# Kernel optimization log

Hardware: AMD Instinct MI355X
Metric: run time of the kernel (lower is better)

Reference implementation:

```python
import jax, jax.numpy as jnp
import numpy as np

DIM = 192
NUM_HEADS = 6
WH, WW = 7, 7
N = WH * WW  # 49 tokens per window
C2 = 2 * DIM  # concatenated channel dim = 384
SCALE = (DIM // NUM_HEADS) ** -0.5  # module uses dim//num_heads, not C2//num_heads
NW = 64  # number of windows per image
B_ = 2048  # num_windows * batch


def _relative_position_index():
    ch = np.arange(WH)
    cw = np.arange(WW)
    coords = np.stack(np.meshgrid(ch, cw, indexing='ij')).reshape(2, -1)  # [2, N]
    rel = coords[:, :, None] - coords[:, None, :]  # [2, N, N]
    rel = rel.transpose(1, 2, 0).astype(np.int64)  # [N, N, 2]
    rel[..., 0] += WH - 1
    rel[..., 1] += WW - 1
    rel[..., 0] *= 2 * WW - 1
    return jnp.asarray(rel.sum(-1))  # [N, N]

REL_IDX = _relative_position_index()


def setup_inputs() -> dict:
    key = jax.random.key(0)
    ks = jax.random.split(key, 8)
    x = jax.random.normal(ks[0], (B_, N, DIM), dtype=jnp.float32)
    y = jax.random.normal(ks[1], (B_, N, DIM), dtype=jnp.float32)
    mask = jax.random.normal(ks[2], (NW, N, N), dtype=jnp.float32)
    w_qkv = jax.random.normal(ks[3], (6 * DIM, C2), dtype=jnp.float32) * 0.02
    b_qkv = jnp.zeros((6 * DIM,), dtype=jnp.float32)
    w_proj = jax.random.normal(ks[4], (DIM, C2), dtype=jnp.float32) * 0.02
    b_proj = jnp.zeros((DIM,), dtype=jnp.float32)
    bias_table = jax.random.normal(ks[5], ((2 * WH - 1) * (2 * WW - 1), NUM_HEADS), dtype=jnp.float32) * 0.02
    return {"x": x, "y": y, "mask": mask, "w_qkv": w_qkv, "b_qkv": b_qkv,
            "w_proj": w_proj, "b_proj": b_proj, "bias_table": bias_table}


def reference(x, y, mask, w_qkv, b_qkv, w_proj, b_proj, bias_table):
    Bc = x.shape[0]
    Dh = C2 // NUM_HEADS  # 64
    xy = jnp.concatenate([x, y], axis=2)  # [B_, N, 2*dim]
    qkv = xy @ w_qkv.T + b_qkv  # [B_, N, 6*dim]
    qkv = qkv.reshape(Bc, N, 3, NUM_HEADS, Dh).transpose(2, 0, 3, 1, 4)  # [3, B_, H, N, Dh]
    q, k, v = qkv[0] * SCALE, qkv[1], qkv[2]
    attn = jnp.einsum('bhnd,bhmd->bhnm', q, k)  # [B_, H, N, N]
    rpb = bias_table[REL_IDX]  # [N, N, H]
    attn = attn + rpb.transpose(2, 0, 1)[None]
    nW = mask.shape[0]
    attn = attn.reshape(Bc // nW, nW, NUM_HEADS, N, N) + mask[None, :, None]
    attn = attn.reshape(Bc, NUM_HEADS, N, N)
    attn = jax.nn.softmax(attn, axis=-1)
    out = jnp.einsum('bhnm,bhmd->bhnd', attn, v)  # [B_, H, N, Dh]
    out = out.transpose(0, 2, 1, 3).reshape(Bc, N, C2)
    return out @ w_proj.T + b_proj  # [B_, N, dim]
```

## Files before the change

kernel.cpp:

```cpp
#include <hip/hip_runtime.h>
#include <hip/hip_bf16.h>


typedef __attribute__((ext_vector_type(8))) short short8;
typedef __attribute__((ext_vector_type(4))) float f32x4;

#define SCALE 0.17677669529663687f

#define WQF_OFF    0ul
#define WQF_BYTES  (864ul*1024)
#define WPF_OFF    (WQF_OFF + WQF_BYTES)
#define WPF_BYTES  (144ul*1024)
#define COMB_OFF   (WPF_OFF + WPF_BYTES)
#define COMB_BYTES (64ul*6*4096*4)
#define XYF_OFF    (COMB_OFF + COMB_BYTES)
#define XYF_BYTES  (2048ul*48*1024)
#define OF_OFF     (XYF_OFF + XYF_BYTES)
#define OF_BYTES   XYF_BYTES
#define WS_NEED    (OF_OFF + OF_BYTES)

__device__ __forceinline__ unsigned short f2bf(float f){
  unsigned u = __builtin_bit_cast(unsigned, f);
  u = u + 0x7fffu + ((u >> 16) & 1u);
  return (unsigned short)(u >> 16);
}
__device__ __forceinline__ unsigned long long pack4(float4 v){
  return (unsigned long long)f2bf(v.x) | ((unsigned long long)f2bf(v.y) << 16)
       | ((unsigned long long)f2bf(v.z) << 32) | ((unsigned long long)f2bf(v.w) << 48);
}

__device__ __forceinline__ unsigned short cvt1(float x){
  unsigned r;
  asm("v_cvt_pk_bf16_f32 %0, %1, %1" : "=v"(r) : "v"(x));
  return (unsigned short)r;
}
__device__ __forceinline__ uint2 pk4(float a, float b, float c, float d){
  unsigned lo, hi;
  asm("v_cvt_pk_bf16_f32 %0, %1, %2" : "=v"(lo) : "v"(a), "v"(b));
  asm("v_cvt_pk_bf16_f32 %0, %1, %2" : "=v"(hi) : "v"(c), "v"(d));
  return make_uint2(lo, hi);
}

__global__ void k0_wfrag(const float* __restrict__ wq_f, const float* __restrict__ wp_f,
                         unsigned short* __restrict__ wqf, unsigned short* __restrict__ wpf){
  int t = blockIdx.x*256 + threadIdx.x;
  int fragidx = t >> 6, l = t & 63;
  const float* src; unsigned short* dst;
  float sc = 1.0f;
  if (fragidx < 864){
    int h = fragidx/144, rem = fragidx - h*144;
    int ct = rem/12, kt = rem - ct*12;
    int row = (ct>>2)*384 + h*64 + (ct&3)*16 + (l&15);
    src = wq_f + (long)row*384 + kt*32 + (l>>4)*8;
    dst = wqf + (long)fragidx*512 + l*8;
    if (ct < 4) sc = SCALE;
  } else {
    int fid = fragidx - 864;
    int ct = fid/12, kt = fid - ct*12;
    int row = ct*16 + (l&15);
    src = wp_f + (long)row*384 + kt*32 + (l>>4)*8;
    dst = wpf + (long)fid*512 + l*8;
  }
  short8 v;
  #pragma unroll
  for (int e = 0; e < 8; ++e) v[e] = (short)f2bf(src[e] * sc);
  *(short8*)dst = v;
}

__global__ void prep_comb(const float* __restrict__ mask, const float* __restrict__ btab,
                          float* __restrict__ comb){
  int idx = blockIdx.x * 256 + threadIdx.x;
  int j = idx & 63, i = (idx >> 6) & 63, rest = idx >> 12;
  int h = rest % 6, w = rest / 6;
  float v;
  if (i < 49 && j < 49){
    int di = i / 7 - j / 7 + 6;
    int dj = i % 7 - j % 7 + 6;
    v = btab[(di * 13 + dj) * 6 + h] + mask[(w * 49 + i) * 49 + j];
  } else {
    v = (j >= 49) ? -1e30f : 0.0f;
  }
  comb[idx] = v;
}

__global__ void k1_xyfrag(const float* __restrict__ x, const float* __restrict__ y,
                          unsigned short* __restrict__ xyf){
  const int kt  = blockIdx.x;
  const int win = blockIdx.y;
  const int mt  = threadIdx.x >> 6;
  const int l   = threadIdx.x & 63;
  const int row = mt*16 + (l & 15);
  const int c0  = kt*32 + (l >> 4)*8;
  short8 v = {};
  if (row < 49){
    const float* src = (kt < 6) ? (x + ((long)win*49 + row)*192 + c0)
                                : (y + ((long)win*49 + row)*192 + (c0 - 192));
    float4 f0 = *(const float4*)src, f1 = *(const float4*)(src+4);
    unsigned long long lo = pack4(f0), hi = pack4(f1);
    #pragma unroll
    for (int e = 0; e < 4; ++e){ v[e] = (short)(lo >> (16*e)); v[4+e] = (short)(hi >> (16*e)); }
  }
  *(short8*)(xyf + (((long)win*12 + kt)*4 + mt)*512 + l*8) = v;
}

__device__ __forceinline__ int swz(int r, int b){ return b ^ ((r & 7) << 4); }
__device__ __forceinline__ int a_q (int r, int c){ return 0     + swz(r, r*128 + c*2); }
__device__ __forceinline__ int a_k (int r, int c){ return 8192  + swz(r, r*128 + c*2); }
__device__ __forceinline__ int a_vt(int r, int c){ return 16384 + swz(r, r*128 + c*2); }

__global__ __launch_bounds__(256, 3)
void k2_qkv_attn(const unsigned short* __restrict__ xyf, const unsigned short* __restrict__ wqf,
                 const float* __restrict__ bqkv, const float* __restrict__ comb,
                 unsigned short* __restrict__ Of){
  __shared__ __align__(16) unsigned char smem[24576];
  const int h = blockIdx.x, win = blockIdx.y;
  const int tid = threadIdx.x, w = tid>>6, l = tid&63, l15 = l&15, lg = l>>4;

  float bias[3];
  #pragma unroll
  for (int nt = 0; nt < 3; ++nt){
    int ct = w*3 + nt, s = ct >> 2;
    bias[nt] = bqkv[s*384 + h*64 + (ct & 3)*16 + l15];
    if (s == 0) bias[nt] *= SCALE;
  }

  const unsigned short* Ab = xyf + (long)win*24576;
  const unsigned short* Bb = wqf + ((long)h*12 + w*3)*12*512;
  short8 aA[2][4], bB[2][3];
  #pragma unroll
  for (int mt = 0; mt < 4; ++mt) aA[0][mt] = *(const short8*)(Ab + mt*512 + l*8);
  #pragma unroll
  for (int nt = 0; nt < 3; ++nt) bB[0][nt] = *(const short8*)(Bb + (nt*12)*512 + l*8);

  f32x4 acc[4][3];
  #pragma unroll
  for (int mt = 0; mt < 4; ++mt)
    #pragma unroll
    for (int nt = 0; nt < 3; ++nt)
      #pragma unroll
      for (int j = 0; j < 4; ++j) acc[mt][nt][j] = bias[nt];

  #pragma unroll
  for (int kt = 0; kt < 12; ++kt){
    const int cur = kt & 1, nxt = cur ^ 1;
    if (kt < 11){
      #pragma unroll
      for (int mt = 0; mt < 4; ++mt)
        aA[nxt][mt] = *(const short8*)(Ab + ((kt+1)*4 + mt)*512 + l*8);
      #pragma unroll
      for (int nt = 0; nt < 3; ++nt)
        bB[nxt][nt] = *(const short8*)(Bb + (nt*12 + kt+1)*512 + l*8);
    }
    __builtin_amdgcn_sched_barrier(0);
    __builtin_amdgcn_s_setprio(1);
    #pragma unroll
    for (int nt = 0; nt < 3; ++nt){
      #pragma unroll
      for (int mt = 0; mt < 4; ++mt)
        acc[mt][nt] = __builtin_amdgcn_mfma_f32_16x16x32_bf16(aA[cur][mt], bB[cur][nt], acc[mt][nt], 0, 0, 0);
    }
    __builtin_amdgcn_s_setprio(0);
  }

  const float* cb = comb + ((long)((win & 63)*6 + h))*4096 + (w*16 + l15)*64 + lg*4;
  float4 cbv[4];
  #pragma unroll
  for (int nt = 0; nt < 4; ++nt) cbv[nt] = *(const float4*)(cb + nt*16);

  #pragma unroll
  for (int nt = 0; nt < 3; ++nt){
    int ct = w*3 + nt, s = ct >> 2, d16 = (ct & 3) * 16;
    if (s == 2){
      #pragma unroll
      for (int mt = 0; mt < 4; ++mt){
        uint2 p = pk4(acc[mt][nt][0], acc[mt][nt][1], acc[mt][nt][2], acc[mt][nt][3]);
        *(uint2*)(smem + a_vt(d16 + l15, mt*16 + lg*4)) = p;
      }
    } else {
      #pragma unroll
      for (int mt = 0; mt < 4; ++mt){
        #pragma unroll
        for (int j = 0; j < 4; ++j){
          int row = mt*16 + lg*4 + j;
          int addr = (s == 0) ? a_q(row, d16 + l15) : a_k(row, d16 + l15);
          *(unsigned short*)(smem + addr) = cvt1(acc[mt][nt][j]);
        }
      }
    }
  }
  __syncthreads();

  short8 bq[2];
  #pragma unroll
  for (int ks = 0; ks < 2; ++ks)
    bq[ks] = *(const short8*)(smem + a_q(w*16 + l15, ks*32 + lg*8));
  f32x4 st[4] = {};
  __builtin_amdgcn_s_setprio(1);
  #pragma unroll
  for (int ks = 0; ks < 2; ++ks){
    #pragma unroll
    for (int nt = 0; nt < 4; ++nt){
      short8 ak = *(const short8*)(smem + a_k(nt*16 + l15, ks*32 + lg*8));
      st[nt] = __builtin_amdgcn_mfma_f32_16x16x32_bf16(ak, bq[ks], st[nt], 0, 0, 0);
    }
  }
  __builtin_amdgcn_s_setprio(0);
  #pragma unroll
  for (int nt = 0; nt < 4; ++nt){
    st[nt][0] += cbv[nt].x; st[nt][1] += cbv[nt].y;
    st[nt][2] += cbv[nt].z; st[nt][3] += cbv[nt].w;
  }
  float mx;
  {
    float m0 = fmaxf(fmaxf(st[0][0], st[0][1]), fmaxf(st[0][2], st[0][3]));
    float m1 = fmaxf(fmaxf(st[1][0], st[1][1]), fmaxf(st[1][2], st[1][3]));
    float m2 = fmaxf(fmaxf(st[2][0], st[2][1]), fmaxf(st[2][2], st[2][3]));
    float m3 = fmaxf(fmaxf(st[3][0], st[3][1]), fmaxf(st[3][2], st[3][3]));
    mx = fmaxf(fmaxf(m0, m1), fmaxf(m2, m3));
  }
  mx = fmaxf(mx, __shfl_xor(mx, 16));
  mx = fmaxf(mx, __shfl_xor(mx, 32));
  float ssum = 0.f;
  #pragma unroll
  for (int nt = 0; nt < 4; ++nt){
    #pragma unroll
    for (int j = 0; j < 4; ++j){
      float e = __expf(st[nt][j] - mx);
      st[nt][j] = e; ssum += e;
    }
  }
  ssum += __shfl_xor(ssum, 16);
  ssum += __shfl_xor(ssum, 32);
  const float inv = 1.0f / ssum;

  #pragma unroll
  for (int nt = 0; nt < 4; ++nt){
    uint2 p = pk4(st[nt][0]*inv, st[nt][1]*inv, st[nt][2]*inv, st[nt][3]*inv);
    *(uint2*)(smem + a_q(w*16 + l15, nt*16 + lg*4)) = p;
  }

  short8 ap[2];
  #pragma unroll
  for (int ks = 0; ks < 2; ++ks)
    ap[ks] = *(const short8*)(smem + a_q(w*16 + l15, ks*32 + lg*8));
  f32x4 oacc[4] = {};
  __builtin_amdgcn_s_setprio(1);
  #pragma unroll
  for (int ks = 0; ks < 2; ++ks){
    #pragma unroll
    for (int nt = 0; nt < 4; ++nt){
      short8 bv = *(const short8*)(smem + a_vt(nt*16 + l15, ks*32 + lg*8));
      oacc[nt] = __builtin_amdgcn_mfma_f32_16x16x32_bf16(ap[ks], bv, oacc[nt], 0, 0, 0);
    }
  }
  __builtin_amdgcn_s_setprio(0);
  #pragma unroll
  for (int nt = 0; nt < 4; ++nt){
    #pragma unroll
    for (int j = 0; j < 4; ++j)
      *(unsigned short*)(smem + a_q(w*16 + lg*4 + j, nt*16 + l15)) = cvt1(oacc[nt][j]);
  }
  unsigned short* Ob = Of + (((long)win*12 + h*2)*4 + w)*512 + l*8;
  #pragma unroll
  for (int ks = 0; ks < 2; ++ks){
    short8 o8 = *(const short8*)(smem + a_q(w*16 + l15, ks*32 + lg*8));
    *(short8*)(Ob + ks*4*512) = o8;
  }
}

__global__ __launch_bounds__(256, 3)
void k3_proj(const unsigned short* __restrict__ Of, const unsigned short* __restrict__ wpf,
             const float* __restrict__ bproj, float* __restrict__ out){
  const int win = blockIdx.x;
  const int tid = threadIdx.x, w = tid>>6, l = tid&63, l15 = l&15, lg = l>>4;
  float bp[3]; int np[3];
  #pragma unroll
  for (int nt = 0; nt < 3; ++nt){
    np[nt] = w*48 + nt*16 + l15;
    bp[nt] = bproj[np[nt]];
  }
  const unsigned short* Ab = Of + (long)win*24576;
  const unsigned short* Bb = wpf + (long)(w*3)*12*512;
  short8 aA[2][4], bB[2][3];
  #pragma unroll
  for (int mt = 0; mt < 4; ++mt) aA[0][mt] = *(const short8*)(Ab + mt*512 + l*8);
  #pragma unroll
  for (int nt = 0; nt < 3; ++nt) bB[0][nt] = *(const short8*)(Bb + (nt*12)*512 + l*8);
  f32x4 acc[4][3];
  #pragma unroll
  for (int mt = 0; mt < 4; ++mt)
    #pragma unroll
    for (int nt = 0; nt < 3; ++nt)
      #pragma unroll
      for (int j = 0; j < 4; ++j) acc[mt][nt][j] = bp[nt];
  #pragma unroll
  for (int kt = 0; kt < 12; ++kt){
    const int cur = kt & 1, nxt = cur ^ 1;
    if (kt < 11){
      #pragma unroll
      for (int mt = 0; mt < 4; ++mt)
        aA[nxt][mt] = *(const short8*)(Ab + ((kt+1)*4 + mt)*512 + l*8);
      #pragma unroll
      for (int nt = 0; nt < 3; ++nt)
        bB[nxt][nt] = *(const short8*)(Bb + (nt*12 + kt+1)*512 + l*8);
    }
    __builtin_amdgcn_sched_barrier(0);
    __builtin_amdgcn_s_setprio(1);
    #pragma unroll
    for (int nt = 0; nt < 3; ++nt){
      #pragma unroll
      for (int mt = 0; mt < 4; ++mt)
        acc[mt][nt] = __builtin_amdgcn_mfma_f32_16x16x32_bf16(aA[cur][mt], bB[cur][nt], acc[mt][nt], 0, 0, 0);
    }
    __builtin_amdgcn_s_setprio(0);
  }
  #pragma unroll
  for (int mt = 0; mt < 4; ++mt){
    #pragma unroll
    for (int j = 0; j < 4; ++j){
      int row = mt*16 + lg*4 + j;
      if (row < 49){
        float* o = out + ((long)win*49 + row)*192;
        #pragma unroll
        for (int nt = 0; nt < 3; ++nt)
          o[np[nt]] = acc[mt][nt][j];
      }
    }
  }
}

#define FB_WQ_ELEMS (1152*384)
#define FB_WP_ELEMS (192*384)
#define FB_WP_OFF   (FB_WQ_ELEMS*2)
#define FB_COMB_OFF (FB_WP_OFF + FB_WP_ELEMS*2)

__global__ void prep_weights_fb(const float* __restrict__ wq_f, const float* __restrict__ wp_f,
                                unsigned short* __restrict__ wq, unsigned short* __restrict__ wp){
  int gid = blockIdx.x * 256 + threadIdx.x;
  if (gid < FB_WQ_ELEMS) wq[gid] = f2bf(wq_f[gid]);
  else { int g = gid - FB_WQ_ELEMS; if (g < FB_WP_ELEMS) wp[g] = f2bf(wp_f[g]); }
}
__device__ __forceinline__ int fb_xy(int r, int c){ return 0      + swz(r, r*768 + c*2); }
__device__ __forceinline__ int fb_q (int r, int c){ return 49152  + swz(r, r*128 + c*2); }
__device__ __forceinline__ int fb_k (int r, int c){ return 57344  + swz(r, r*128 + c*2); }
__device__ __forceinline__ int fb_vt(int r, int c){ return 65536  + swz(r, r*128 + c*2); }
__device__ __forceinline__ int fb_p (int r, int c){ return 73728  + swz(r, r*128 + c*2); }

__global__ __launch_bounds__(256, 2)
void fused_attn_fb(const float* __restrict__ x, const float* __restrict__ y,
                   const float* __restrict__ bqkv, const float* __restrict__ bproj,
                   const unsigned short* __restrict__ wq, const unsigned short* __restrict__ wp,
                   const float* __restrict__ comb, float* __restrict__ out){
  __shared__ __align__(16) unsigned char smem[81920];
  const int b = blockIdx.x, tid = threadIdx.x;
  const int w = tid>>6, l = tid&63, l15 = l&15, lg = l>>4;
  {
    const float4* x4 = (const float4*)x + b * 2352;
    const float4* y4 = (const float4*)y + b * 2352;
    for (int idx = tid; idx < 2352; idx += 256){
      int r = idx / 48, c4 = (idx % 48) * 4;
      float4 vx = x4[idx], vy = y4[idx];
      *(unsigned long long*)(smem + fb_xy(r, c4))       = pack4(vx);
      *(unsigned long long*)(smem + fb_xy(r, 192 + c4)) = pack4(vy);
    }
    for (int idx = tid; idx < 1440; idx += 256){
      int r = 49 + idx / 96, c4 = (idx % 96) * 4;
      *(unsigned long long*)(smem + fb_xy(r, c4)) = 0ull;
    }
  }
  __syncthreads();
  const float* cbB = comb + (long)(b & 63) * (6 * 4096);
  f32x4 pacc[4][3] = {};
  int np[3]; float bp[3];
  #pragma unroll
  for (int nt = 0; nt < 3; ++nt){ np[nt] = w*48 + nt*16 + l15; bp[nt] = bproj[np[nt]]; }
  #pragma unroll 1
  for (int h = 0; h < 6; ++h){
    f32x4 acc[4][3] = {};
    int wrow[3]; float bias[3];
    #pragma unroll
    for (int nt = 0; nt < 3; ++nt){
      int n = np[nt];
      wrow[nt] = (n >> 6) * 384 + h * 64 + (n & 63);
      bias[nt] = bqkv[wrow[nt]];
    }
    #pragma unroll 4
    for (int kt = 0; kt < 12; ++kt){
      int k0 = kt * 32;
      short8 a[4];
      #pragma unroll
      for (int mt = 0; mt < 4; ++mt)
        a[mt] = *(const short8*)(smem + fb_xy(mt*16 + l15, k0 + lg*8));
      #pragma unroll
      for (int nt = 0; nt < 3; ++nt){
        short8 bb = *(const short8*)(wq + (long)wrow[nt]*384 + k0 + lg*8);
        #pragma unroll
        for (int mt = 0; mt < 4; ++mt)
          acc[mt][nt] = __builtin_amdgcn_mfma_f32_16x16x32_bf16(a[mt], bb, acc[mt][nt], 0, 0, 0);
      }
    }
    #pragma unroll
    for (int nt = 0; nt < 3; ++nt){
      int n = np[nt], s = n >> 6, d = n & 63;
      #pragma unroll
      for (int mt = 0; mt < 4; ++mt){
        #pragma unroll
        for (int j = 0; j < 4; ++j){
          int row = mt*16 + lg*4 + j;
          float v = acc[mt][nt][j] + bias[nt];
          if (s == 0) v *= SCALE;
          int addr = (s==0) ? fb_q(row,d) : (s==1) ? fb_k(row,d) : fb_vt(d,row);
          *(unsigned short*)(smem + addr) = f2bf(v);
        }
      }
    }
    __syncthreads();
    short8 aq[2];
    #pragma unroll
    for (int ks = 0; ks < 2; ++ks)
      aq[ks] = *(const short8*)(smem + fb_q(w*16 + l15, ks*32 + lg*8));
    f32x4 sacc[4] = {};
    #pragma unroll
    for (int ks = 0; ks < 2; ++ks)
      #pragma unroll
      for (int nt = 0; nt < 4; ++nt){
        short8 bk = *(const short8*)(smem + fb_k(nt*16 + l15, ks*32 + lg*8));
        sacc[nt] = __builtin_amdgcn_mfma_f32_16x16x32_bf16(aq[ks], bk, sacc[nt], 0, 0, 0);
      }
    const float* cb = cbB + h * 4096;
    float rs[4];
    #pragma unroll
    for (int j = 0; j < 4; ++j){
      int r = w*16 + lg*4 + j;
      #pragma unroll
      for (int nt = 0; nt < 4; ++nt) sacc[nt][j] += cb[r*64 + nt*16 + l15];
      float m = fmaxf(fmaxf(sacc[0][j], sacc[1][j]), fmaxf(sacc[2][j], sacc[3][j]));
      #pragma unroll
      for (int dlt = 1; dlt < 16; dlt <<= 1) m = fmaxf(m, __shfl_xor(m, dlt));
      float ssum = 0.f;
      #pragma unroll
      for (int nt = 0; nt < 4; ++nt){
        float e = __expf(sacc[nt][j] - m);
        sacc[nt][j] = e; ssum += e;
      }
      #pragma unroll
      for (int dlt = 1; dlt < 16; dlt <<= 1) ssum += __shfl_xor(ssum, dlt);
      rs[j] = ssum;
      #pragma unroll
      for (int nt = 0; nt < 4; ++nt)
        *(unsigned short*)(smem + fb_p(r, nt*16 + l15)) = f2bf(sacc[nt][j]);
    }
    short8 ap[2];
    #pragma unroll
    for (int ks = 0; ks < 2; ++ks)
      ap[ks] = *(const short8*)(smem + fb_p(w*16 + l15, ks*32 + lg*8));
    f32x4 oacc[4] = {};
    #pragma unroll
    for (int ks = 0; ks < 2; ++ks)
      #pragma unroll
      for (int nt = 0; nt < 4; ++nt){
        short8 bv = *(const short8*)(smem + fb_vt(nt*16 + l15, ks*32 + lg*8));
        oacc[nt] = __builtin_amdgcn_mfma_f32_16x16x32_bf16(ap[ks], bv, oacc[nt], 0, 0, 0);
      }
    float inv[4];
    #pragma unroll
    for (int j = 0; j < 4; ++j) inv[j] = 1.0f / rs[j];
    #pragma unroll
    for (int nt = 0; nt < 4; ++nt)
      #pragma unroll
      for (int j = 0; j < 4; ++j){
        int row = w*16 + lg*4 + j;
        *(unsigned short*)(smem + fb_p(row, nt*16 + l15)) = f2bf(oacc[nt][j] * inv[j]);
      }
    __syncthreads();
    #pragma unroll
    for (int ks = 0; ks < 2; ++ks){
      short8 ao8[4];
      #pragma unroll
      for (int mt = 0; mt < 4; ++mt)
        ao8[mt] = *(const short8*)(smem + fb_p(mt*16 + l15, ks*32 + lg*8));
      #pragma unroll
      for (int nt = 0; nt < 3; ++nt){
        short8 bb = *(const short8*)(wp + (long)np[nt]*384 + h*64 + ks*32 + lg*8);
        #pragma unroll
        for (int mt = 0; mt < 4; ++mt)
          pacc[mt][nt] = __builtin_amdgcn_mfma_f32_16x16x32_bf16(ao8[mt], bb, pacc[mt][nt], 0, 0, 0);
      }
    }
  }
  #pragma unroll
  for (int mt = 0; mt < 4; ++mt)
    #pragma unroll
    for (int j = 0; j < 4; ++j){
      int row = mt*16 + lg*4 + j;
      if (row < 49){
        float* o = out + ((long)b*49 + row)*192;
        #pragma unroll
        for (int nt = 0; nt < 3; ++nt)
          o[np[nt]] = pacc[mt][nt][j] + bp[nt];
      }
    }
}

extern "C" void kernel_launch(void* const* d_in, const int* in_sizes, int n_in,
                              void* d_out, int out_size, void* d_ws, size_t ws_size,
                              hipStream_t stream){
  (void)in_sizes; (void)n_in; (void)out_size;
  const float* x     = (const float*)d_in[0];
  const float* y     = (const float*)d_in[1];
  const float* mask  = (const float*)d_in[2];
  const float* wq_f  = (const float*)d_in[3];
  const float* bqkv  = (const float*)d_in[4];
  const float* wp_f  = (const float*)d_in[5];
  const float* bproj = (const float*)d_in[6];
  const float* btab  = (const float*)d_in[7];
  float* out = (float*)d_out;

  if (ws_size >= WS_NEED){
    unsigned short* wqf = (unsigned short*)((char*)d_ws + WQF_OFF);
    unsigned short* wpf = (unsigned short*)((char*)d_ws + WPF_OFF);
    float*          cmb = (float*)((char*)d_ws + COMB_OFF);
    unsigned short* xyf = (unsigned short*)((char*)d_ws + XYF_OFF);
    unsigned short* Ofr = (unsigned short*)((char*)d_ws + OF_OFF);
    hipLaunchKernelGGL(k0_wfrag,    dim3(252),     dim3(256), 0, stream, wq_f, wp_f, wqf, wpf);
    hipLaunchKernelGGL(prep_comb,   dim3(6144),    dim3(256), 0, stream, mask, btab, cmb);
    hipLaunchKernelGGL(k1_xyfrag,   dim3(12,2048), dim3(256), 0, stream, x, y, xyf);
    hipLaunchKernelGGL(k2_qkv_attn, dim3(6,2048),  dim3(256), 0, stream, xyf, wqf, bqkv, cmb, Ofr);
    hipLaunchKernelGGL(k3_proj,     dim3(2048),    dim3(256), 0, stream, Ofr, wpf, bproj, out);
  } else {
    unsigned short* wq  = (unsigned short*)d_ws;
    unsigned short* wp  = (unsigned short*)((char*)d_ws + FB_WP_OFF);
    float*          cmb = (float*)((char*)d_ws + FB_COMB_OFF);
    hipLaunchKernelGGL(prep_weights_fb, dim3(2016), dim3(256), 0, stream, wq_f, wp_f, wq, wp);
    hipLaunchKernelGGL(prep_comb,       dim3(6144), dim3(256), 0, stream, mask, btab, cmb);
    hipLaunchKernelGGL(fused_attn_fb,   dim3(2048), dim3(256), 0, stream,
                       x, y, bqkv, bproj, wq, wp, cmb, out);
  }
}
```

Baseline: 251.6 us.

## Fuse input conversion, per-head QKV attention and projection into one kernel per window

```diff
diff --git a/kernel.cpp b/kernel.cpp
--- a/kernel.cpp
+++ b/kernel.cpp
@@ -13,11 +13,7 @@
 #define WPF_BYTES  (144ul*1024)
 #define COMB_OFF   (WPF_OFF + WPF_BYTES)
 #define COMB_BYTES (64ul*6*4096*4)
-#define XYF_OFF    (COMB_OFF + COMB_BYTES)
-#define XYF_BYTES  (2048ul*48*1024)
-#define OF_OFF     (XYF_OFF + XYF_BYTES)
-#define OF_BYTES   XYF_BYTES
-#define WS_NEED    (OF_OFF + OF_BYTES)
+#define WS_NEED    (COMB_OFF + COMB_BYTES)
 
 __device__ __forceinline__ unsigned short f2bf(float f){
   unsigned u = __builtin_bit_cast(unsigned, f);
@@ -83,237 +79,229 @@
   comb[idx] = v;
 }
 
-__global__ void k1_xyfrag(const float* __restrict__ x, const float* __restrict__ y,
-                          unsigned short* __restrict__ xyf){
-  const int kt  = blockIdx.x;
-  const int win = blockIdx.y;
-  const int mt  = threadIdx.x >> 6;
-  const int l   = threadIdx.x & 63;
-  const int row = mt*16 + (l & 15);
-  const int c0  = kt*32 + (l >> 4)*8;
-  short8 v = {};
-  if (row < 49){
-    const float* src = (kt < 6) ? (x + ((long)win*49 + row)*192 + c0)
-                                : (y + ((long)win*49 + row)*192 + (c0 - 192));
-    float4 f0 = *(const float4*)src, f1 = *(const float4*)(src+4);
-    unsigned long long lo = pack4(f0), hi = pack4(f1);
-    #pragma unroll
-    for (int e = 0; e < 4; ++e){ v[e] = (short)(lo >> (16*e)); v[4+e] = (short)(hi >> (16*e)); }
-  }
-  *(short8*)(xyf + (((long)win*12 + kt)*4 + mt)*512 + l*8) = v;
-}
-
 __device__ __forceinline__ int swz(int r, int b){ return b ^ ((r & 7) << 4); }
-__device__ __forceinline__ int a_q (int r, int c){ return 0     + swz(r, r*128 + c*2); }
-__device__ __forceinline__ int a_k (int r, int c){ return 8192  + swz(r, r*128 + c*2); }
-__device__ __forceinline__ int a_vt(int r, int c){ return 16384 + swz(r, r*128 + c*2); }
-
-__global__ __launch_bounds__(256, 3)
-void k2_qkv_attn(const unsigned short* __restrict__ xyf, const unsigned short* __restrict__ wqf,
-                 const float* __restrict__ bqkv, const float* __restrict__ comb,
-                 unsigned short* __restrict__ Of){
-  __shared__ __align__(16) unsigned char smem[24576];
-  const int h = blockIdx.x, win = blockIdx.y;
-  const int tid = threadIdx.x, w = tid>>6, l = tid&63, l15 = l&15, lg = l>>4;
-
-  float bias[3];
-  #pragma unroll
-  for (int nt = 0; nt < 3; ++nt){
-    int ct = w*3 + nt, s = ct >> 2;
-    bias[nt] = bqkv[s*384 + h*64 + (ct & 3)*16 + l15];
-    if (s == 0) bias[nt] *= SCALE;
-  }
-
-  const unsigned short* Ab = xyf + (long)win*24576;
-  const unsigned short* Bb = wqf + ((long)h*12 + w*3)*12*512;
-  short8 aA[2][4], bB[2][3];
-  #pragma unroll
-  for (int mt = 0; mt < 4; ++mt) aA[0][mt] = *(const short8*)(Ab + mt*512 + l*8);
-  #pragma unroll
-  for (int nt = 0; nt < 3; ++nt) bB[0][nt] = *(const short8*)(Bb + (nt*12)*512 + l*8);
-
-  f32x4 acc[4][3];
-  #pragma unroll
-  for (int mt = 0; mt < 4; ++mt)
-    #pragma unroll
-    for (int nt = 0; nt < 3; ++nt)
-      #pragma unroll
-      for (int j = 0; j < 4; ++j) acc[mt][nt][j] = bias[nt];
-
-  #pragma unroll
-  for (int kt = 0; kt < 12; ++kt){
-    const int cur = kt & 1, nxt = cur ^ 1;
-    if (kt < 11){
-      #pragma unroll
-      for (int mt = 0; mt < 4; ++mt)
-        aA[nxt][mt] = *(const short8*)(Ab + ((kt+1)*4 + mt)*512 + l*8);
-      #pragma unroll
-      for (int nt = 0; nt < 3; ++nt)
-        bB[nxt][nt] = *(const short8*)(Bb + (nt*12 + kt+1)*512 + l*8);
-    }
-    __builtin_amdgcn_sched_barrier(0);
-    __builtin_amdgcn_s_setprio(1);
-    #pragma unroll
-    for (int nt = 0; nt < 3; ++nt){
-      #pragma unroll
-      for (int mt = 0; mt < 4; ++mt)
-        acc[mt][nt] = __builtin_amdgcn_mfma_f32_16x16x32_bf16(aA[cur][mt], bB[cur][nt], acc[mt][nt], 0, 0, 0);
-    }
-    __builtin_amdgcn_s_setprio(0);
-  }
-
-  const float* cb = comb + ((long)((win & 63)*6 + h))*4096 + (w*16 + l15)*64 + lg*4;
-  float4 cbv[4];
-  #pragma unroll
-  for (int nt = 0; nt < 4; ++nt) cbv[nt] = *(const float4*)(cb + nt*16);
-
-  #pragma unroll
-  for (int nt = 0; nt < 3; ++nt){
-    int ct = w*3 + nt, s = ct >> 2, d16 = (ct & 3) * 16;
-    if (s == 2){
-      #pragma unroll
-      for (int mt = 0; mt < 4; ++mt){
-        uint2 p = pk4(acc[mt][nt][0], acc[mt][nt][1], acc[mt][nt][2], acc[mt][nt][3]);
-        *(uint2*)(smem + a_vt(d16 + l15, mt*16 + lg*4)) = p;
-      }
-    } else {
-      #pragma unroll
-      for (int mt = 0; mt < 4; ++mt){
-        #pragma unroll
-        for (int j = 0; j < 4; ++j){
-          int row = mt*16 + lg*4 + j;
-          int addr = (s == 0) ? a_q(row, d16 + l15) : a_k(row, d16 + l15);
-          *(unsigned short*)(smem + addr) = cvt1(acc[mt][nt][j]);
-        }
-      }
-    }
-  }
-  __syncthreads();
-
-  short8 bq[2];
-  #pragma unroll
-  for (int ks = 0; ks < 2; ++ks)
-    bq[ks] = *(const short8*)(smem + a_q(w*16 + l15, ks*32 + lg*8));
-  f32x4 st[4] = {};
-  __builtin_amdgcn_s_setprio(1);
-  #pragma unroll
-  for (int ks = 0; ks < 2; ++ks){
-    #pragma unroll
-    for (int nt = 0; nt < 4; ++nt){
-      short8 ak = *(const short8*)(smem + a_k(nt*16 + l15, ks*32 + lg*8));
-      st[nt] = __builtin_amdgcn_mfma_f32_16x16x32_bf16(ak, bq[ks], st[nt], 0, 0, 0);
-    }
-  }
-  __builtin_amdgcn_s_setprio(0);
-  #pragma unroll
-  for (int nt = 0; nt < 4; ++nt){
-    st[nt][0] += cbv[nt].x; st[nt][1] += cbv[nt].y;
-    st[nt][2] += cbv[nt].z; st[nt][3] += cbv[nt].w;
-  }
-  float mx;
-  {
-    float m0 = fmaxf(fmaxf(st[0][0], st[0][1]), fmaxf(st[0][2], st[0][3]));
-    float m1 = fmaxf(fmaxf(st[1][0], st[1][1]), fmaxf(st[1][2], st[1][3]));
-    float m2 = fmaxf(fmaxf(st[2][0], st[2][1]), fmaxf(st[2][2], st[2][3]));
-    float m3 = fmaxf(fmaxf(st[3][0], st[3][1]), fmaxf(st[3][2], st[3][3]));
-    mx = fmaxf(fmaxf(m0, m1), fmaxf(m2, m3));
-  }
-  mx = fmaxf(mx, __shfl_xor(mx, 16));
-  mx = fmaxf(mx, __shfl_xor(mx, 32));
-  float ssum = 0.f;
-  #pragma unroll
-  for (int nt = 0; nt < 4; ++nt){
-    #pragma unroll
-    for (int j = 0; j < 4; ++j){
-      float e = __expf(st[nt][j] - mx);
-      st[nt][j] = e; ssum += e;
-    }
-  }
-  ssum += __shfl_xor(ssum, 16);
-  ssum += __shfl_xor(ssum, 32);
-  const float inv = 1.0f / ssum;
-
-  #pragma unroll
-  for (int nt = 0; nt < 4; ++nt){
-    uint2 p = pk4(st[nt][0]*inv, st[nt][1]*inv, st[nt][2]*inv, st[nt][3]*inv);
-    *(uint2*)(smem + a_q(w*16 + l15, nt*16 + lg*4)) = p;
-  }
-
-  short8 ap[2];
-  #pragma unroll
-  for (int ks = 0; ks < 2; ++ks)
-    ap[ks] = *(const short8*)(smem + a_q(w*16 + l15, ks*32 + lg*8));
-  f32x4 oacc[4] = {};
-  __builtin_amdgcn_s_setprio(1);
-  #pragma unroll
-  for (int ks = 0; ks < 2; ++ks){
-    #pragma unroll
-    for (int nt = 0; nt < 4; ++nt){
-      short8 bv = *(const short8*)(smem + a_vt(nt*16 + l15, ks*32 + lg*8));
-      oacc[nt] = __builtin_amdgcn_mfma_f32_16x16x32_bf16(ap[ks], bv, oacc[nt], 0, 0, 0);
-    }
-  }
-  __builtin_amdgcn_s_setprio(0);
-  #pragma unroll
-  for (int nt = 0; nt < 4; ++nt){
-    #pragma unroll
-    for (int j = 0; j < 4; ++j)
-      *(unsigned short*)(smem + a_q(w*16 + lg*4 + j, nt*16 + l15)) = cvt1(oacc[nt][j]);
-  }
-  unsigned short* Ob = Of + (((long)win*12 + h*2)*4 + w)*512 + l*8;
-  #pragma unroll
-  for (int ks = 0; ks < 2; ++ks){
-    short8 o8 = *(const short8*)(smem + a_q(w*16 + l15, ks*32 + lg*8));
-    *(short8*)(Ob + ks*4*512) = o8;
-  }
-}
-
-__global__ __launch_bounds__(256, 3)
-void k3_proj(const unsigned short* __restrict__ Of, const unsigned short* __restrict__ wpf,
-             const float* __restrict__ bproj, float* __restrict__ out){
+__device__ __forceinline__ int a_q (int r, int c){ return 49152 + swz(r, r*128 + c*2); }
+__device__ __forceinline__ int a_k (int r, int c){ return 57344 + swz(r, r*128 + c*2); }
+__device__ __forceinline__ int a_vt(int r, int c){ return 65536 + swz(r, r*128 + c*2); }
+#define OBUF 73728
+
+__global__ __launch_bounds__(256, 2)
+void k_fused(const float* __restrict__ x, const float* __restrict__ y,
+             const unsigned short* __restrict__ wqf, const unsigned short* __restrict__ wpf,
+             const float* __restrict__ bqkv, const float* __restrict__ bproj,
+             const float* __restrict__ comb, float* __restrict__ out){
+  __shared__ __align__(16) unsigned char smem[81920];
   const int win = blockIdx.x;
   const int tid = threadIdx.x, w = tid>>6, l = tid&63, l15 = l&15, lg = l>>4;
-  float bp[3]; int np[3];
+
+  for (int t = tid; t < 2352; t += 256){
+    int r = t / 48, c8 = t - r*48;
+    int c = c8*8;
+    const float* src = (c < 192) ? (x + ((long)win*49 + r)*192 + c)
+                                 : (y + ((long)win*49 + r)*192 + (c - 192));
+    float4 f0 = *(const float4*)src, f1 = *(const float4*)(src + 4);
+    uint2 lo = pk4(f0.x, f0.y, f0.z, f0.w);
+    uint2 hi = pk4(f1.x, f1.y, f1.z, f1.w);
+    uint4 vv = make_uint4(lo.x, lo.y, hi.x, hi.y);
+    int addr = (c8>>2)*4096 + (r>>4)*1024 + (((r&15) + (c8&3)*16))*16;
+    *(uint4*)(smem + addr) = vv;
+  }
+  for (int t = tid; t < 720; t += 256){
+    int rr = t / 48, c8 = t - rr*48;
+    int r = 49 + rr;
+    int addr = (c8>>2)*4096 + (r>>4)*1024 + (((r&15) + (c8&3)*16))*16;
+    *(uint4*)(smem + addr) = make_uint4(0,0,0,0);
+  }
+
+  int np[3];
+  f32x4 pacc[4][3];
   #pragma unroll
   for (int nt = 0; nt < 3; ++nt){
     np[nt] = w*48 + nt*16 + l15;
-    bp[nt] = bproj[np[nt]];
-  }
-  const unsigned short* Ab = Of + (long)win*24576;
-  const unsigned short* Bb = wpf + (long)(w*3)*12*512;
-  short8 aA[2][4], bB[2][3];
+    float bv = bproj[np[nt]];
+    #pragma unroll
+    for (int mt = 0; mt < 4; ++mt)
+      #pragma unroll
+      for (int j = 0; j < 4; ++j) pacc[mt][nt][j] = (mt == 0 && j == 0) ? bv : ((mt==0&&j==0)?bv:0.0f);
+  }
   #pragma unroll
-  for (int mt = 0; mt < 4; ++mt) aA[0][mt] = *(const short8*)(Ab + mt*512 + l*8);
-  #pragma unroll
-  for (int nt = 0; nt < 3; ++nt) bB[0][nt] = *(const short8*)(Bb + (nt*12)*512 + l*8);
-  f32x4 acc[4][3];
-  #pragma unroll
-  for (int mt = 0; mt < 4; ++mt)
-    #pragma unroll
-    for (int nt = 0; nt < 3; ++nt)
-      #pragma unroll
-      for (int j = 0; j < 4; ++j) acc[mt][nt][j] = bp[nt];
-  #pragma unroll
-  for (int kt = 0; kt < 12; ++kt){
-    const int cur = kt & 1, nxt = cur ^ 1;
-    if (kt < 11){
+  for (int nt = 0; nt < 3; ++nt){
+    float bv = bproj[np[nt]];
+    #pragma unroll
+    for (int mt = 0; mt < 4; ++mt)
+      #pragma unroll
+      for (int j = 0; j < 4; ++j) pacc[mt][nt][j] = bv;
+  }
+
+  __syncthreads();
+
+  #pragma unroll 1
+  for (int h = 0; h < 6; ++h){
+    const float* cb = comb + ((long)((win & 63)*6 + h))*4096 + (w*16 + l15)*64 + lg*4;
+    float4 cbv[4];
+    #pragma unroll
+    for (int nt = 0; nt < 4; ++nt) cbv[nt] = *(const float4*)(cb + nt*16);
+
+    float bias[3];
+    #pragma unroll
+    for (int nt = 0; nt < 3; ++nt){
+      int ct = w*3 + nt, s = ct >> 2;
+      bias[nt] = bqkv[s*384 + h*64 + (ct & 3)*16 + l15];
+      if (s == 0) bias[nt] *= SCALE;
+    }
+
+    const unsigned short* Bb = wqf + ((long)h*12 + w*3)*12*512;
+    short8 bB[2][3];
+    #pragma unroll
+    for (int nt = 0; nt < 3; ++nt) bB[0][nt] = *(const short8*)(Bb + (nt*12)*512 + l*8);
+    f32x4 acc[4][3];
+    #pragma unroll
+    for (int mt = 0; mt < 4; ++mt)
+      #pragma unroll
+      for (int nt = 0; nt < 3; ++nt)
+        #pragma unroll
+        for (int j = 0; j < 4; ++j) acc[mt][nt][j] = bias[nt];
+
+    #pragma unroll
+    for (int kt = 0; kt < 12; ++kt){
+      const int cur = kt & 1, nxt = cur ^ 1;
+      if (kt < 11){
+        #pragma unroll
+        for (int nt = 0; nt < 3; ++nt)
+          bB[nxt][nt] = *(const short8*)(Bb + (nt*12 + kt+1)*512 + l*8);
+      }
+      short8 aA[4];
       #pragma unroll
       for (int mt = 0; mt < 4; ++mt)
-        aA[nxt][mt] = *(const short8*)(Ab + ((kt+1)*4 + mt)*512 + l*8);
-      #pragma unroll
-      for (int nt = 0; nt < 3; ++nt)
-        bB[nxt][nt] = *(const short8*)(Bb + (nt*12 + kt+1)*512 + l*8);
-    }
-    __builtin_amdgcn_sched_barrier(0);
+        aA[mt] = *(const short8*)(smem + (kt*4 + mt)*1024 + l*16);
+      __builtin_amdgcn_sched_barrier(0);
+      __builtin_amdgcn_s_setprio(1);
+      #pragma unroll
+      for (int nt = 0; nt < 3; ++nt){
+        #pragma unroll
+        for (int mt = 0; mt < 4; ++mt)
+          acc[mt][nt] = __builtin_amdgcn_mfma_f32_16x16x32_bf16(aA[mt], bB[cur][nt], acc[mt][nt], 0, 0, 0);
+      }
+      __builtin_amdgcn_s_setprio(0);
+    }
+
+    #pragma unroll
+    for (int nt = 0; nt < 3; ++nt){
+      int ct = w*3 + nt, s = ct >> 2, d16 = (ct & 3) * 16;
+      if (s == 2){
+        #pragma unroll
+        for (int mt = 0; mt < 4; ++mt){
+          uint2 p = pk4(acc[mt][nt][0], acc[mt][nt][1], acc[mt][nt][2], acc[mt][nt][3]);
+          *(uint2*)(smem + a_vt(d16 + l15, mt*16 + lg*4)) = p;
+        }
+      } else {
+        #pragma unroll
+        for (int mt = 0; mt < 4; ++mt){
+          #pragma unroll
+          for (int j = 0; j < 4; ++j){
+            int row = mt*16 + lg*4 + j;
+            int addr = (s == 0) ? a_q(row, d16 + l15) : a_k(row, d16 + l15);
+            *(unsigned short*)(smem + addr) = cvt1(acc[mt][nt][j]);
+          }
+        }
+      }
+    }
+    __syncthreads();
+
+    short8 bq[2];
+    #pragma unroll
+    for (int ks = 0; ks < 2; ++ks)
+      bq[ks] = *(const short8*)(smem + a_q(w*16 + l15, ks*32 + lg*8));
+    f32x4 st[4] = {};
     __builtin_amdgcn_s_setprio(1);
     #pragma unroll
-    for (int nt = 0; nt < 3; ++nt){
+    for (int ks = 0; ks < 2; ++ks){
+      #pragma unroll
+      for (int nt = 0; nt < 4; ++nt){
+        short8 ak = *(const short8*)(smem + a_k(nt*16 + l15, ks*32 + lg*8));
+        st[nt] = __builtin_amdgcn_mfma_f32_16x16x32_bf16(ak, bq[ks], st[nt], 0, 0, 0);
+      }
+    }
+    __builtin_amdgcn_s_setprio(0);
+    #pragma unroll
+    for (int nt = 0; nt < 4; ++nt){
+      st[nt][0] += cbv[nt].x; st[nt][1] += cbv[nt].y;
+      st[nt][2] += cbv[nt].z; st[nt][3] += cbv[nt].w;
+    }
+    float mx;
+    {
+      float m0 = fmaxf(fmaxf(st[0][0], st[0][1]), fmaxf(st[0][2], st[0][3]));
+      float m1 = fmaxf(fmaxf(st[1][0], st[1][1]), fmaxf(st[1][2], st[1][3]));
+      float m2 = fmaxf(fmaxf(st[2][0], st[2][1]), fmaxf(st[2][2], st[2][3]));
+      float m3 = fmaxf(fmaxf(st[3][0], st[3][1]), fmaxf(st[3][2], st[3][3]));
+      mx = fmaxf(fmaxf(m0, m1), fmaxf(m2, m3));
+    }
+    mx = fmaxf(mx, __shfl_xor(mx, 16));
+    mx = fmaxf(mx, __shfl_xor(mx, 32));
+    float ssum = 0.f;
+    #pragma unroll
+    for (int nt = 0; nt < 4; ++nt){
+      #pragma unroll
+      for (int j = 0; j < 4; ++j){
+        float e = __expf(st[nt][j] - mx);
+        st[nt][j] = e; ssum += e;
+      }
+    }
+    ssum += __shfl_xor(ssum, 16);
+    ssum += __shfl_xor(ssum, 32);
+    const float inv = 1.0f / ssum;
+
+    #pragma unroll
+    for (int nt = 0; nt < 4; ++nt){
+      uint2 p = pk4(st[nt][0]*inv, st[nt][1]*inv, st[nt][2]*inv, st[nt][3]*inv);
+      *(uint2*)(smem + a_q(w*16 + l15, nt*16 + lg*4)) = p;
+    }
+
+    short8 ap[2];
+    #pragma unroll
+    for (int ks = 0; ks < 2; ++ks)
+      ap[ks] = *(const short8*)(smem + a_q(w*16 + l15, ks*32 + lg*8));
+    f32x4 oacc[4] = {};
+    __builtin_amdgcn_s_setprio(1);
+    #pragma unroll
+    for (int ks = 0; ks < 2; ++ks){
+      #pragma unroll
+      for (int nt = 0; nt < 4; ++nt){
+        short8 bv = *(const short8*)(smem + a_vt(nt*16 + l15, ks*32 + lg*8));
+        oacc[nt] = __builtin_amdgcn_mfma_f32_16x16x32_bf16(ap[ks], bv, oacc[nt], 0, 0, 0);
+      }
+    }
+    __builtin_amdgcn_s_setprio(0);
+    #pragma unroll
+    for (int nt = 0; nt < 4; ++nt){
+      int frag  = (nt >> 1)*4 + w;
+      int chunk0 = (lg*4) + ((nt & 1)*2 + (l15 >> 3))*16;
+      #pragma unroll
+      for (int j = 0; j < 4; ++j){
+        int addr = OBUF + frag*1024 + (chunk0 + j)*16 + (l15 & 7)*2;
+        *(unsigned short*)(smem + addr) = cvt1(oacc[nt][j]);
+      }
+    }
+    __syncthreads();
+
+    #pragma unroll
+    for (int ks = 0; ks < 2; ++ks){
+      short8 aO[4];
       #pragma unroll
       for (int mt = 0; mt < 4; ++mt)
-        acc[mt][nt] = __builtin_amdgcn_mfma_f32_16x16x32_bf16(aA[cur][mt], bB[cur][nt], acc[mt][nt], 0, 0, 0);
-    }
-    __builtin_amdgcn_s_setprio(0);
-  }
+        aO[mt] = *(const short8*)(smem + OBUF + (ks*4 + mt)*1024 + l*16);
+      __builtin_amdgcn_s_setprio(1);
+      #pragma unroll
+      for (int nt = 0; nt < 3; ++nt){
+        short8 bb = *(const short8*)(wpf + ((long)(w*3 + nt)*12 + h*2 + ks)*512 + l*8);
+        #pragma unroll
+        for (int mt = 0; mt < 4; ++mt)
+          pacc[mt][nt] = __builtin_amdgcn_mfma_f32_16x16x32_bf16(aO[mt], bb, pacc[mt][nt], 0, 0, 0);
+      }
+      __builtin_amdgcn_s_setprio(0);
+    }
+  }
+
   #pragma unroll
   for (int mt = 0; mt < 4; ++mt){
     #pragma unroll
@@ -323,7 +311,7 @@
         float* o = out + ((long)win*49 + row)*192;
         #pragma unroll
         for (int nt = 0; nt < 3; ++nt)
-          o[np[nt]] = acc[mt][nt][j];
+          o[np[nt]] = pacc[mt][nt][j];
       }
     }
   }
@@ -520,13 +508,10 @@
     unsigned short* wqf = (unsigned short*)((char*)d_ws + WQF_OFF);
     unsigned short* wpf = (unsigned short*)((char*)d_ws + WPF_OFF);
     float*          cmb = (float*)((char*)d_ws + COMB_OFF);
-    unsigned short* xyf = (unsigned short*)((char*)d_ws + XYF_OFF);
-    unsigned short* Ofr = (unsigned short*)((char*)d_ws + OF_OFF);
-    hipLaunchKernelGGL(k0_wfrag,    dim3(252),     dim3(256), 0, stream, wq_f, wp_f, wqf, wpf);
-    hipLaunchKernelGGL(prep_comb,   dim3(6144),    dim3(256), 0, stream, mask, btab, cmb);
-    hipLaunchKernelGGL(k1_xyfrag,   dim3(12,2048), dim3(256), 0, stream, x, y, xyf);
-    hipLaunchKernelGGL(k2_qkv_attn, dim3(6,2048),  dim3(256), 0, stream, xyf, wqf, bqkv, cmb, Ofr);
-    hipLaunchKernelGGL(k3_proj,     dim3(2048),    dim3(256), 0, stream, Ofr, wpf, bproj, out);
+    hipLaunchKernelGGL(k0_wfrag,  dim3(252),  dim3(256), 0, stream, wq_f, wp_f, wqf, wpf);
+    hipLaunchKernelGGL(prep_comb, dim3(6144), dim3(256), 0, stream, mask, btab, cmb);
+    hipLaunchKernelGGL(k_fused,   dim3(2048), dim3(256), 0, stream,
+                       x, y, wqf, wpf, bqkv, bproj, cmb, out);
   } else {
     unsigned short* wq  = (unsigned short*)d_ws;
     unsigned short* wp  = (unsigned short*)((char*)d_ws + FB_WP_OFF);
```

New measurement: 220.9 us. 12.2% less time.
